# Kernel tuning notes

Hardware: AMD Instinct MI355X
Metric: run time of the kernel (lower is better)

Reference implementation:

```python
import jax, jax.numpy as jnp
import numpy as np

DIM = 512
HEADS = 8
HEAD_DIM = DIM // HEADS
MLP_HIDDEN = int(DIM * 4.0)
B, N = 4, 2048
LS_INIT = 1e-5
EPS = 1e-5


def _layernorm(x, w, b):
    mu = jnp.mean(x, axis=-1, keepdims=True)
    var = jnp.mean(jnp.square(x - mu), axis=-1, keepdims=True)
    return (x - mu) * jax.lax.rsqrt(var + EPS) * w + b


def setup_inputs() -> dict:
    key = jax.random.key(0)
    ks = jax.random.split(key, 12)
    s = 0.02
    return {
        "x": jax.random.normal(ks[0], (B, N, DIM), jnp.float32),
        "rel_pos_bias": jax.random.normal(ks[1], (HEADS, N, N), jnp.float32),
        "qkv_w": jax.random.normal(ks[2], (DIM, 3 * DIM), jnp.float32) * s,
        "qkv_b": jnp.zeros((3 * DIM,), jnp.float32),
        "out_w": jax.random.normal(ks[3], (DIM, DIM), jnp.float32) * s,
        "out_b": jnp.zeros((DIM,), jnp.float32),
        "ln1_w": jnp.ones((DIM,), jnp.float32),
        "ln1_b": jnp.zeros((DIM,), jnp.float32),
        "ln2_w": jnp.ones((DIM,), jnp.float32),
        "ln2_b": jnp.zeros((DIM,), jnp.float32),
        "ffn_w1": jax.random.normal(ks[4], (DIM, MLP_HIDDEN), jnp.float32) * s,
        "ffn_b1": jnp.zeros((MLP_HIDDEN,), jnp.float32),
        "ffn_w2": jax.random.normal(ks[5], (MLP_HIDDEN, DIM), jnp.float32) * s,
        "ffn_b2": jnp.zeros((DIM,), jnp.float32),
        "gamma1": jnp.full((DIM,), LS_INIT, jnp.float32),
        "gamma2": jnp.full((DIM,), LS_INIT, jnp.float32),
    }


def reference(x, rel_pos_bias, qkv_w, qkv_b, out_w, out_b, ln1_w, ln1_b,
              ln2_w, ln2_b, ffn_w1, ffn_b1, ffn_w2, ffn_b2, gamma1, gamma2):
    # Pre-norm MHA with relative-position bias
    y = _layernorm(x, ln1_w, ln1_b)                       # [B,N,C]
    qkv = y @ qkv_w + qkv_b                               # [B,N,3C]
    qkv = qkv.reshape(B, N, 3, HEADS, HEAD_DIM)
    q = jnp.transpose(qkv[:, :, 0], (0, 2, 1, 3))         # [B,H,N,D]
    k = jnp.transpose(qkv[:, :, 1], (0, 2, 1, 3))
    v = jnp.transpose(qkv[:, :, 2], (0, 2, 1, 3))
    scale = 1.0 / np.sqrt(HEAD_DIM).astype(np.float32)
    attn = jnp.einsum("bhid,bhjd->bhij", q, k) * scale    # [B,H,N,N]
    attn = attn + rel_pos_bias[None]
    attn = jax.nn.softmax(attn, axis=-1)
    out = jnp.einsum("bhij,bhjd->bhid", attn, v)          # [B,H,N,D]
    out = jnp.transpose(out, (0, 2, 1, 3)).reshape(B, N, DIM)
    out = out @ out_w + out_b
    x = x + out * gamma1                                  # layer scale, no drop-path (eval)
    # FFN with exact GELU
    y2 = _layernorm(x, ln2_w, ln2_b)
    h = jax.nn.gelu(y2 @ ffn_w1 + ffn_b1, approximate=False)
    ffn_out = h @ ffn_w2 + ffn_b2
    x = x + ffn_out * gamma2
    return x
```

## Files before the change

### kernel.cpp

```cpp
#include <hip/hip_runtime.h>
#include <hip/hip_bf16.h>
#include <math.h>

#define SEQ 2048
#define BATCH 4
#define DM 512
#define NH 8
#define HD 64
#define HID 2048
#define ROWS (BATCH * SEQ)

typedef __attribute__((ext_vector_type(8))) short short8;
typedef __attribute__((ext_vector_type(4))) float f32x4;

__device__ __forceinline__ short f2bf(float f) {
    unsigned u = __float_as_uint(f);
    u += 0x7fff + ((u >> 16) & 1);
    return (short)(u >> 16);
}

__global__ __launch_bounds__(256) void tcast_k(const float* __restrict__ W,
                                               short* __restrict__ Wt,
                                               int K, int N) {
    __shared__ float tile[32][33];
    int tx = threadIdx.x, ty = threadIdx.y;
    int n0 = blockIdx.x * 32, k0 = blockIdx.y * 32;
#pragma unroll
    for (int i = 0; i < 4; ++i)
        tile[ty + i * 8][tx] = W[(size_t)(k0 + ty + i * 8) * N + n0 + tx];
    __syncthreads();
#pragma unroll
    for (int i = 0; i < 4; ++i)
        Wt[(size_t)(n0 + ty + i * 8) * K + k0 + tx] = f2bf(tile[tx][ty + i * 8]);
}

__global__ __launch_bounds__(256) void ln_k(const float* __restrict__ X,
                                            const float* __restrict__ g,
                                            const float* __restrict__ bta,
                                            short* __restrict__ Y) {
    int t = threadIdx.x;
    int wv = t >> 6, ln = t & 63;
    size_t row = (size_t)blockIdx.x * 4 + wv;
    const float* xr = X + row * DM;
    float4 v0 = *(const float4*)(xr + ln * 4);
    float4 v1 = *(const float4*)(xr + 256 + ln * 4);
    float s = v0.x + v0.y + v0.z + v0.w + v1.x + v1.y + v1.z + v1.w;
    float q = v0.x * v0.x + v0.y * v0.y + v0.z * v0.z + v0.w * v0.w +
              v1.x * v1.x + v1.y * v1.y + v1.z * v1.z + v1.w * v1.w;
#pragma unroll
    for (int off = 1; off < 64; off <<= 1) {
        s += __shfl_xor(s, off);
        q += __shfl_xor(q, off);
    }
    float mean = s * (1.0f / 512.0f);
    float var = q * (1.0f / 512.0f) - mean * mean;
    float rstd = rsqrtf(var + 1e-5f);
    int c0 = ln * 4, c1 = 256 + ln * 4;
    ushort4 o0, o1;
    o0.x = (unsigned short)f2bf((v0.x - mean) * rstd * g[c0 + 0] + bta[c0 + 0]);
    o0.y = (unsigned short)f2bf((v0.y - mean) * rstd * g[c0 + 1] + bta[c0 + 1]);
    o0.z = (unsigned short)f2bf((v0.z - mean) * rstd * g[c0 + 2] + bta[c0 + 2]);
    o0.w = (unsigned short)f2bf((v0.w - mean) * rstd * g[c0 + 3] + bta[c0 + 3]);
    o1.x = (unsigned short)f2bf((v1.x - mean) * rstd * g[c1 + 0] + bta[c1 + 0]);
    o1.y = (unsigned short)f2bf((v1.y - mean) * rstd * g[c1 + 1] + bta[c1 + 1]);
    o1.z = (unsigned short)f2bf((v1.z - mean) * rstd * g[c1 + 2] + bta[c1 + 2]);
    o1.w = (unsigned short)f2bf((v1.w - mean) * rstd * g[c1 + 3] + bta[c1 + 3]);
    *(ushort4*)((unsigned short*)Y + row * DM + c0) = o0;
    *(ushort4*)((unsigned short*)Y + row * DM + c1) = o1;
}

template <int EPI>
__global__ __launch_bounds__(256) void gemm_bt(const short* __restrict__ A,
                                               const short* __restrict__ Bt,
                                               const float* __restrict__ bias,
                                               const float* __restrict__ gamma,
                                               const float* __restrict__ res,
                                               void* __restrict__ Cout,
                                               int M, int N, int K) {
    __shared__ short As[128][40];
    __shared__ short Bs[128][40];
    int t = threadIdx.x;
    int w = t >> 6, ln = t & 63;
    int quad = ln >> 4, l15 = ln & 15;
    int n0 = blockIdx.x * 128, m0 = blockIdx.y * 128;
    int wm = (w & 1) * 64, wn = (w >> 1) * 64;

    int rA0 = t >> 2;
    int cA0 = (t & 3) * 8;

    f32x4 acc[4][4];
#pragma unroll
    for (int i = 0; i < 4; ++i)
#pragma unroll
        for (int j = 0; j < 4; ++j) acc[i][j] = (f32x4){0.f, 0.f, 0.f, 0.f};

    for (int k0 = 0; k0 < K; k0 += 32) {
        float4 av0 = *(const float4*)(A + (size_t)(m0 + rA0) * K + k0 + cA0);
        float4 av1 = *(const float4*)(A + (size_t)(m0 + rA0 + 64) * K + k0 + cA0);
        float4 bv0 = *(const float4*)(Bt + (size_t)(n0 + rA0) * K + k0 + cA0);
        float4 bv1 = *(const float4*)(Bt + (size_t)(n0 + rA0 + 64) * K + k0 + cA0);
        __syncthreads();
        *(float4*)&As[rA0][cA0] = av0;
        *(float4*)&As[rA0 + 64][cA0] = av1;
        *(float4*)&Bs[rA0][cA0] = bv0;
        *(float4*)&Bs[rA0 + 64][cA0] = bv1;
        __syncthreads();
        short8 af[4], bf[4];
#pragma unroll
        for (int mi = 0; mi < 4; ++mi)
            af[mi] = *(const short8*)&As[wm + mi * 16 + l15][quad * 8];
#pragma unroll
        for (int ni = 0; ni < 4; ++ni)
            bf[ni] = *(const short8*)&Bs[wn + ni * 16 + l15][quad * 8];
#pragma unroll
        for (int mi = 0; mi < 4; ++mi)
#pragma unroll
            for (int ni = 0; ni < 4; ++ni)
                acc[mi][ni] = __builtin_amdgcn_mfma_f32_16x16x32_bf16(
                    af[mi], bf[ni], acc[mi][ni], 0, 0, 0);
    }

#pragma unroll
    for (int mi = 0; mi < 4; ++mi) {
#pragma unroll
        for (int ni = 0; ni < 4; ++ni) {
#pragma unroll
            for (int r = 0; r < 4; ++r) {
                int row = m0 + wm + mi * 16 + quad * 4 + r;
                int col = n0 + wn + ni * 16 + l15;
                float v = acc[mi][ni][r] + bias[col];
                if (EPI == 0) {
                    ((short*)Cout)[(size_t)row * N + col] = f2bf(v);
                } else if (EPI == 1) {
                    float gg = 0.5f * v * (1.0f + erff(v * 0.70710678118654752f));
                    ((short*)Cout)[(size_t)row * N + col] = f2bf(gg);
                } else {
                    ((float*)Cout)[(size_t)row * N + col] =
                        fmaf(v, gamma[col], res[(size_t)row * N + col]);
                }
            }
        }
    }
}

__global__ __launch_bounds__(256) void attn_k(const short* __restrict__ qkv,
                                              const float* __restrict__ bias,
                                              short* __restrict__ Aout) {
    __shared__ short Qs[64][72];
    __shared__ short Ks[64][72];
    __shared__ short Vt[64][72];
    __shared__ short Ps[4][16][72];
    int t = threadIdx.x;
    int w = t >> 6, ln = t & 63, quad = ln >> 4, l15 = ln & 15;
    int idx = blockIdx.x;
    int qt = idx >> 5, bh = idx & 31;
    int h = bh >> 2, b = bh & 3;
    int q0 = qt * 64;
    size_t base = (size_t)b * SEQ * 1536;

    {
        int r0 = t >> 3, c = (t & 7) * 8;
        *(float4*)&Qs[r0][c] =
            *(const float4*)(qkv + base + (size_t)(q0 + r0) * 1536 + h * 64 + c);
        *(float4*)&Qs[r0 + 32][c] =
            *(const float4*)(qkv + base + (size_t)(q0 + r0 + 32) * 1536 + h * 64 + c);
    }
    __syncthreads();
    short8 aq0 = *(const short8*)&Qs[w * 16 + l15][quad * 8];
    short8 aq1 = *(const short8*)&Qs[w * 16 + l15][32 + quad * 8];

    float m_s[4], l_s[4];
    f32x4 o[4];
#pragma unroll
    for (int r = 0; r < 4; ++r) { m_s[r] = -1e30f; l_s[r] = 0.f; }
#pragma unroll
    for (int db = 0; db < 4; ++db) o[db] = (f32x4){0.f, 0.f, 0.f, 0.f};

    const float sc = 0.125f;
    for (int jt = 0; jt < 32; ++jt) {
        int j0 = jt * 64;
        __syncthreads();
        {
            int r0 = t >> 3, c = (t & 7) * 8;
            *(float4*)&Ks[r0][c] = *(const float4*)(qkv + base +
                (size_t)(j0 + r0) * 1536 + 512 + h * 64 + c);
            *(float4*)&Ks[r0 + 32][c] = *(const float4*)(qkv + base +
                (size_t)(j0 + r0 + 32) * 1536 + 512 + h * 64 + c);
            int kp = r0;
            union { float4 f; short8 s; } ua, ub;
            ua.f = *(const float4*)(qkv + base + (size_t)(j0 + 2 * kp) * 1536 + 1024 + h * 64 + c);
            ub.f = *(const float4*)(qkv + base + (size_t)(j0 + 2 * kp + 1) * 1536 + 1024 + h * 64 + c);
#pragma unroll
            for (int j = 0; j < 8; ++j) {
                ushort2 pr;
                pr.x = (unsigned short)ua.s[j];
                pr.y = (unsigned short)ub.s[j];
                *(ushort2*)&Vt[c + j][2 * kp] = pr;
            }
        }
        __syncthreads();
        f32x4 s[4];
#pragma unroll
        for (int ni = 0; ni < 4; ++ni) {
            s[ni] = (f32x4){0.f, 0.f, 0.f, 0.f};
            short8 bk0 = *(const short8*)&Ks[ni * 16 + l15][quad * 8];
            short8 bk1 = *(const short8*)&Ks[ni * 16 + l15][32 + quad * 8];
            s[ni] = __builtin_amdgcn_mfma_f32_16x16x32_bf16(aq0, bk0, s[ni], 0, 0, 0);
            s[ni] = __builtin_amdgcn_mfma_f32_16x16x32_bf16(aq1, bk1, s[ni], 0, 0, 0);
        }
        const float* bp = bias + (size_t)h * SEQ * SEQ +
                          (size_t)(q0 + w * 16 + quad * 4) * SEQ + j0 + l15;
        float sv[4][4];
#pragma unroll
        for (int r = 0; r < 4; ++r) {
#pragma unroll
            for (int ni = 0; ni < 4; ++ni)
                sv[ni][r] = s[ni][r] * sc + bp[(size_t)r * SEQ + ni * 16];
            float mx = fmaxf(fmaxf(sv[0][r], sv[1][r]), fmaxf(sv[2][r], sv[3][r]));
#pragma unroll
            for (int off = 1; off < 16; off <<= 1) mx = fmaxf(mx, __shfl_xor(mx, off));
            float mn = fmaxf(m_s[r], mx);
            float alpha = __expf(m_s[r] - mn);
            m_s[r] = mn;
            float rs = 0.f;
#pragma unroll
            for (int ni = 0; ni < 4; ++ni) {
                float p = __expf(sv[ni][r] - mn);
                sv[ni][r] = p;
                rs += p;
            }
#pragma unroll
            for (int off = 1; off < 16; off <<= 1) rs += __shfl_xor(rs, off);
            l_s[r] = l_s[r] * alpha + rs;
#pragma unroll
            for (int db = 0; db < 4; ++db) o[db][r] *= alpha;
#pragma unroll
            for (int ni = 0; ni < 4; ++ni)
                Ps[w][quad * 4 + r][ni * 16 + l15] = f2bf(sv[ni][r]);
        }
        __syncthreads();
#pragma unroll
        for (int kk = 0; kk < 2; ++kk) {
            short8 ap = *(const short8*)&Ps[w][l15][kk * 32 + quad * 8];
#pragma unroll
            for (int db = 0; db < 4; ++db) {
                short8 bv = *(const short8*)&Vt[db * 16 + l15][kk * 32 + quad * 8];
                o[db] = __builtin_amdgcn_mfma_f32_16x16x32_bf16(ap, bv, o[db], 0, 0, 0);
            }
        }
    }
#pragma unroll
    for (int db = 0; db < 4; ++db)
#pragma unroll
        for (int r = 0; r < 4; ++r) {
            float v = o[db][r] / l_s[r];
            Aout[(size_t)(b * SEQ + q0 + w * 16 + quad * 4 + r) * DM +
                 h * 64 + db * 16 + l15] = f2bf(v);
        }
}

extern "C" void kernel_launch(void* const* d_in, const int* in_sizes, int n_in,
                              void* d_out, int out_size, void* d_ws, size_t ws_size,
                              hipStream_t stream) {
    const float* x      = (const float*)d_in[0];
    const float* bias   = (const float*)d_in[1];
    const float* qkv_w  = (const float*)d_in[2];
    const float* qkv_b  = (const float*)d_in[3];
    const float* out_w  = (const float*)d_in[4];
    const float* out_b  = (const float*)d_in[5];
    const float* ln1_w  = (const float*)d_in[6];
    const float* ln1_b  = (const float*)d_in[7];
    const float* ln2_w  = (const float*)d_in[8];
    const float* ln2_b  = (const float*)d_in[9];
    const float* ffn_w1 = (const float*)d_in[10];
    const float* ffn_b1 = (const float*)d_in[11];
    const float* ffn_w2 = (const float*)d_in[12];
    const float* ffn_b2 = (const float*)d_in[13];
    const float* gamma1 = (const float*)d_in[14];
    const float* gamma2 = (const float*)d_in[15];
    float* out = (float*)d_out;

    short* wqkvT = (short*)d_ws;
    short* woutT = wqkvT + (size_t)1536 * 512;
    short* w1T   = woutT + (size_t)512 * 512;
    short* w2T   = w1T + (size_t)2048 * 512;
    short* y1    = w2T + (size_t)512 * 2048;
    short* qkvB  = y1 + (size_t)ROWS * DM;
    short* aoutB = qkvB + (size_t)ROWS * 1536;
    float* x1    = (float*)(aoutB + (size_t)ROWS * DM);
    short* hB    = qkvB;

    tcast_k<<<dim3(1536 / 32, 512 / 32), dim3(32, 8), 0, stream>>>(qkv_w, wqkvT, 512, 1536);
    tcast_k<<<dim3(512 / 32, 512 / 32), dim3(32, 8), 0, stream>>>(out_w, woutT, 512, 512);
    tcast_k<<<dim3(2048 / 32, 512 / 32), dim3(32, 8), 0, stream>>>(ffn_w1, w1T, 512, 2048);
    tcast_k<<<dim3(512 / 32, 2048 / 32), dim3(32, 8), 0, stream>>>(ffn_w2, w2T, 2048, 512);

    ln_k<<<ROWS / 4, 256, 0, stream>>>(x, ln1_w, ln1_b, y1);
    gemm_bt<0><<<dim3(1536 / 128, ROWS / 128), 256, 0, stream>>>(
        y1, wqkvT, qkv_b, nullptr, nullptr, qkvB, ROWS, 1536, 512);
    attn_k<<<1024, 256, 0, stream>>>(qkvB, bias, aoutB);
    gemm_bt<2><<<dim3(512 / 128, ROWS / 128), 256, 0, stream>>>(
        aoutB, woutT, out_b, gamma1, x, x1, ROWS, 512, 512);
    ln_k<<<ROWS / 4, 256, 0, stream>>>(x1, ln2_w, ln2_b, y1);
    gemm_bt<1><<<dim3(2048 / 128, ROWS / 128), 256, 0, stream>>>(
        y1, w1T, ffn_b1, nullptr, nullptr, hB, ROWS, 2048, 512);
    gemm_bt<2><<<dim3(512 / 128, ROWS / 128), 256, 0, stream>>>(
        hB, w2T, ffn_b2, gamma2, x1, out, ROWS, 512, 2048);
}
```

Measured before the change: 492.1 us.

## Restructure attention with direct LDS bias loads and max-free softmax

The attention kernel now loads Q and K fragments straight into registers and computes the transposed score tile, so its Q/K shared-memory staging goes away. The relative-position bias tile is copied into XOR-swizzled LDS with global_load_lds, the running-max online softmax is dropped, and row sums come from an MFMA against a ones vector. The GEMM also switches to direct global-to-LDS loads with unpadded tiles. Skipping max subtraction removes the shuffles and rescaling, but it can overflow exp for large logits and only stays safe for moderate score ranges.

```diff
diff --git a/kernel.cpp b/kernel.cpp
--- a/kernel.cpp
+++ b/kernel.cpp
@@ -17,6 +17,12 @@
     unsigned u = __float_as_uint(f);
     u += 0x7fff + ((u >> 16) & 1);
     return (short)(u >> 16);
+}
+
+__device__ __forceinline__ void gl2lds16(const void* g, void* l) {
+    __builtin_amdgcn_global_load_lds(
+        (const __attribute__((address_space(1))) void*)g,
+        (__attribute__((address_space(3))) void*)l, 16, 0, 0);
 }
 
 __global__ __launch_bounds__(256) void tcast_k(const float* __restrict__ W,
@@ -77,16 +83,21 @@
                                                const float* __restrict__ res,
                                                void* __restrict__ Cout,
                                                int M, int N, int K) {
-    __shared__ short As[128][40];
-    __shared__ short Bs[128][40];
+    __shared__ __attribute__((aligned(16))) short As[128][32];
+    __shared__ __attribute__((aligned(16))) short Bs[128][32];
     int t = threadIdx.x;
     int w = t >> 6, ln = t & 63;
     int quad = ln >> 4, l15 = ln & 15;
     int n0 = blockIdx.x * 128, m0 = blockIdx.y * 128;
     int wm = (w & 1) * 64, wn = (w >> 1) * 64;
 
-    int rA0 = t >> 2;
-    int cA0 = (t & 3) * 8;
+    int srow0 = w * 32 + (ln >> 2);
+    int srow1 = srow0 + 16;
+    int schunk = (ln & 3) * 8;
+    const short* Ag0 = A + (size_t)(m0 + srow0) * K + schunk;
+    const short* Ag1 = A + (size_t)(m0 + srow1) * K + schunk;
+    const short* Bg0 = Bt + (size_t)(n0 + srow0) * K + schunk;
+    const short* Bg1 = Bt + (size_t)(n0 + srow1) * K + schunk;
 
     f32x4 acc[4][4];
 #pragma unroll
@@ -95,15 +106,11 @@
         for (int j = 0; j < 4; ++j) acc[i][j] = (f32x4){0.f, 0.f, 0.f, 0.f};
 
     for (int k0 = 0; k0 < K; k0 += 32) {
-        float4 av0 = *(const float4*)(A + (size_t)(m0 + rA0) * K + k0 + cA0);
-        float4 av1 = *(const float4*)(A + (size_t)(m0 + rA0 + 64) * K + k0 + cA0);
-        float4 bv0 = *(const float4*)(Bt + (size_t)(n0 + rA0) * K + k0 + cA0);
-        float4 bv1 = *(const float4*)(Bt + (size_t)(n0 + rA0 + 64) * K + k0 + cA0);
         __syncthreads();
-        *(float4*)&As[rA0][cA0] = av0;
-        *(float4*)&As[rA0 + 64][cA0] = av1;
-        *(float4*)&Bs[rA0][cA0] = bv0;
-        *(float4*)&Bs[rA0 + 64][cA0] = bv1;
+        gl2lds16(Ag0 + k0, &As[srow0][schunk]);
+        gl2lds16(Ag1 + k0, &As[srow1][schunk]);
+        gl2lds16(Bg0 + k0, &Bs[srow0][schunk]);
+        gl2lds16(Bg1 + k0, &Bs[srow1][schunk]);
         __syncthreads();
         short8 af[4], bf[4];
 #pragma unroll
@@ -143,120 +150,111 @@
     }
 }
 
-__global__ __launch_bounds__(256) void attn_k(const short* __restrict__ qkv,
-                                              const float* __restrict__ bias,
-                                              short* __restrict__ Aout) {
-    __shared__ short Qs[64][72];
-    __shared__ short Ks[64][72];
-    __shared__ short Vt[64][72];
-    __shared__ short Ps[4][16][72];
+__global__ __launch_bounds__(256, 4) void attn_k(const short* __restrict__ qkv,
+                                                 const float* __restrict__ bias,
+                                                 short* __restrict__ Aout) {
+    __shared__ __attribute__((aligned(16))) short Vt[64][72];
+    __shared__ __attribute__((aligned(16))) short Ps[4][16][72];
+    __shared__ __attribute__((aligned(16))) float Bsf[64 * 64];
     int t = threadIdx.x;
     int w = t >> 6, ln = t & 63, quad = ln >> 4, l15 = ln & 15;
     int idx = blockIdx.x;
     int qt = idx >> 5, bh = idx & 31;
     int h = bh >> 2, b = bh & 3;
     int q0 = qt * 64;
-    size_t base = (size_t)b * SEQ * 1536;
-
-    {
-        int r0 = t >> 3, c = (t & 7) * 8;
-        *(float4*)&Qs[r0][c] =
-            *(const float4*)(qkv + base + (size_t)(q0 + r0) * 1536 + h * 64 + c);
-        *(float4*)&Qs[r0 + 32][c] =
-            *(const float4*)(qkv + base + (size_t)(q0 + r0 + 32) * 1536 + h * 64 + c);
-    }
-    __syncthreads();
-    short8 aq0 = *(const short8*)&Qs[w * 16 + l15][quad * 8];
-    short8 aq1 = *(const short8*)&Qs[w * 16 + l15][32 + quad * 8];
-
-    float m_s[4], l_s[4];
-    f32x4 o[4];
-#pragma unroll
-    for (int r = 0; r < 4; ++r) { m_s[r] = -1e30f; l_s[r] = 0.f; }
+    const size_t base = (size_t)b * SEQ * 1536;
+
+    const short* qrow = qkv + base + (size_t)(q0 + w * 16 + l15) * 1536 + h * 64;
+    short8 qf0 = *(const short8*)(qrow + quad * 8);
+    short8 qf1 = *(const short8*)(qrow + 32 + quad * 8);
+
+    const short* kbase = qkv + base + 512 + h * 64 + (size_t)l15 * 1536 + quad * 8;
+    int kp = t & 31, vc = (t >> 5) * 8;
+    const short* vbase = qkv + base + 1024 + h * 64 + (size_t)(2 * kp) * 1536 + vc;
+    const float* bias_h = bias + (size_t)h * SEQ * SEQ + (size_t)q0 * SEQ;
+
+    short8 ones;
+#pragma unroll
+    for (int i = 0; i < 8; ++i) ones[i] = (short)0x3F80;
+
+    f32x4 o[4], ol;
 #pragma unroll
     for (int db = 0; db < 4; ++db) o[db] = (f32x4){0.f, 0.f, 0.f, 0.f};
-
-    const float sc = 0.125f;
+    ol = (f32x4){0.f, 0.f, 0.f, 0.f};
+
     for (int jt = 0; jt < 32; ++jt) {
         int j0 = jt * 64;
+        short8 kf0[4], kf1[4];
+        const short* kr = kbase + (size_t)j0 * 1536;
+#pragma unroll
+        for (int ni = 0; ni < 4; ++ni) {
+            kf0[ni] = *(const short8*)(kr + ni * 16 * 1536);
+            kf1[ni] = *(const short8*)(kr + ni * 16 * 1536 + 32);
+        }
+        const short* vr = vbase + (size_t)j0 * 1536;
+        union { float4 f; short s[8]; } ua, ub;
+        ua.f = *(const float4*)vr;
+        ub.f = *(const float4*)(vr + 1536);
         __syncthreads();
-        {
-            int r0 = t >> 3, c = (t & 7) * 8;
-            *(float4*)&Ks[r0][c] = *(const float4*)(qkv + base +
-                (size_t)(j0 + r0) * 1536 + 512 + h * 64 + c);
-            *(float4*)&Ks[r0 + 32][c] = *(const float4*)(qkv + base +
-                (size_t)(j0 + r0 + 32) * 1536 + 512 + h * 64 + c);
-            int kp = r0;
-            union { float4 f; short8 s; } ua, ub;
-            ua.f = *(const float4*)(qkv + base + (size_t)(j0 + 2 * kp) * 1536 + 1024 + h * 64 + c);
-            ub.f = *(const float4*)(qkv + base + (size_t)(j0 + 2 * kp + 1) * 1536 + 1024 + h * 64 + c);
-#pragma unroll
-            for (int j = 0; j < 8; ++j) {
-                ushort2 pr;
-                pr.x = (unsigned short)ua.s[j];
-                pr.y = (unsigned short)ub.s[j];
-                *(ushort2*)&Vt[c + j][2 * kp] = pr;
-            }
+#pragma unroll
+        for (int i = 0; i < 4; ++i) {
+            int s = (i * 4 + w) * 64 + ln;
+            int row = s >> 4, pch = s & 15;
+            int lch = pch ^ (row & 15);
+            gl2lds16(bias_h + (size_t)row * SEQ + j0 + lch * 4,
+                     &Bsf[row * 64 + pch * 4]);
+        }
+#pragma unroll
+        for (int j = 0; j < 8; ++j) {
+            ushort2 pr;
+            pr.x = (unsigned short)ua.s[j];
+            pr.y = (unsigned short)ub.s[j];
+            *(ushort2*)&Vt[vc + j][2 * kp] = pr;
         }
         __syncthreads();
-        f32x4 s[4];
+        f32x4 s4[4];
 #pragma unroll
         for (int ni = 0; ni < 4; ++ni) {
-            s[ni] = (f32x4){0.f, 0.f, 0.f, 0.f};
-            short8 bk0 = *(const short8*)&Ks[ni * 16 + l15][quad * 8];
-            short8 bk1 = *(const short8*)&Ks[ni * 16 + l15][32 + quad * 8];
-            s[ni] = __builtin_amdgcn_mfma_f32_16x16x32_bf16(aq0, bk0, s[ni], 0, 0, 0);
-            s[ni] = __builtin_amdgcn_mfma_f32_16x16x32_bf16(aq1, bk1, s[ni], 0, 0, 0);
-        }
-        const float* bp = bias + (size_t)h * SEQ * SEQ +
-                          (size_t)(q0 + w * 16 + quad * 4) * SEQ + j0 + l15;
-        float sv[4][4];
-#pragma unroll
-        for (int r = 0; r < 4; ++r) {
-#pragma unroll
-            for (int ni = 0; ni < 4; ++ni)
-                sv[ni][r] = s[ni][r] * sc + bp[(size_t)r * SEQ + ni * 16];
-            float mx = fmaxf(fmaxf(sv[0][r], sv[1][r]), fmaxf(sv[2][r], sv[3][r]));
-#pragma unroll
-            for (int off = 1; off < 16; off <<= 1) mx = fmaxf(mx, __shfl_xor(mx, off));
-            float mn = fmaxf(m_s[r], mx);
-            float alpha = __expf(m_s[r] - mn);
-            m_s[r] = mn;
-            float rs = 0.f;
-#pragma unroll
-            for (int ni = 0; ni < 4; ++ni) {
-                float p = __expf(sv[ni][r] - mn);
-                sv[ni][r] = p;
-                rs += p;
-            }
-#pragma unroll
-            for (int off = 1; off < 16; off <<= 1) rs += __shfl_xor(rs, off);
-            l_s[r] = l_s[r] * alpha + rs;
-#pragma unroll
-            for (int db = 0; db < 4; ++db) o[db][r] *= alpha;
-#pragma unroll
-            for (int ni = 0; ni < 4; ++ni)
-                Ps[w][quad * 4 + r][ni * 16 + l15] = f2bf(sv[ni][r]);
-        }
-        __syncthreads();
+            s4[ni] = (f32x4){0.f, 0.f, 0.f, 0.f};
+            s4[ni] = __builtin_amdgcn_mfma_f32_16x16x32_bf16(kf0[ni], qf0, s4[ni], 0, 0, 0);
+            s4[ni] = __builtin_amdgcn_mfma_f32_16x16x32_bf16(kf1[ni], qf1, s4[ni], 0, 0, 0);
+        }
+#pragma unroll
+        for (int ni = 0; ni < 4; ++ni) {
+            float4 bb = *(const float4*)&Bsf[(w * 16 + l15) * 64 +
+                                             (((4 * ni + quad) ^ l15) << 2)];
+            float p0 = __expf(fmaf(s4[ni][0], 0.125f, bb.x));
+            float p1 = __expf(fmaf(s4[ni][1], 0.125f, bb.y));
+            float p2 = __expf(fmaf(s4[ni][2], 0.125f, bb.z));
+            float p3 = __expf(fmaf(s4[ni][3], 0.125f, bb.w));
+            ushort4 pk;
+            pk.x = (unsigned short)f2bf(p0);
+            pk.y = (unsigned short)f2bf(p1);
+            pk.z = (unsigned short)f2bf(p2);
+            pk.w = (unsigned short)f2bf(p3);
+            *(ushort4*)&Ps[w][l15][ni * 16 + quad * 4] = pk;
+        }
 #pragma unroll
         for (int kk = 0; kk < 2; ++kk) {
             short8 ap = *(const short8*)&Ps[w][l15][kk * 32 + quad * 8];
 #pragma unroll
             for (int db = 0; db < 4; ++db) {
-                short8 bv = *(const short8*)&Vt[db * 16 + l15][kk * 32 + quad * 8];
-                o[db] = __builtin_amdgcn_mfma_f32_16x16x32_bf16(ap, bv, o[db], 0, 0, 0);
+                short8 vv = *(const short8*)&Vt[db * 16 + l15][kk * 32 + quad * 8];
+                o[db] = __builtin_amdgcn_mfma_f32_16x16x32_bf16(ap, vv, o[db], 0, 0, 0);
             }
-        }
-    }
-#pragma unroll
-    for (int db = 0; db < 4; ++db)
-#pragma unroll
-        for (int r = 0; r < 4; ++r) {
-            float v = o[db][r] / l_s[r];
-            Aout[(size_t)(b * SEQ + q0 + w * 16 + quad * 4 + r) * DM +
-                 h * 64 + db * 16 + l15] = f2bf(v);
-        }
+            ol = __builtin_amdgcn_mfma_f32_16x16x32_bf16(ap, ones, ol, 0, 0, 0);
+        }
+    }
+#pragma unroll
+    for (int r = 0; r < 4; ++r) {
+        float inv = 1.0f / ol[r];
+        int qrow_g = b * SEQ + q0 + w * 16 + quad * 4 + r;
+#pragma unroll
+        for (int db = 0; db < 4; ++db) {
+            Aout[(size_t)qrow_g * DM + h * 64 + db * 16 + l15] =
+                f2bf(o[db][r] * inv);
+        }
+    }
 }
 
 extern "C" void kernel_launch(void* const* d_in, const int* in_sizes, int n_in,
```

New measurement: 533.0 us. 8.3% more time.
